# Kernel optimization log

Measured on AMD Instinct MI355X. Metric: run time of the kernel, lower is better.

Reference implementation:

```python
import jax, jax.numpy as jnp
import numpy as np

HEAD_DIM = 128
NUM_HEADS = 16
NUM_KV_HEADS = 16
ROPE_MAX_POS = 4096
ROPE_BASE = 10000.0


def _rope_tables(seq_len):
    # cos/sin cached tables: [S, D/2]
    inv_freq = 1.0 / (ROPE_BASE ** (jnp.arange(0, HEAD_DIM, 2, dtype=jnp.float32) / HEAD_DIM))
    t = jnp.arange(seq_len, dtype=jnp.float32)
    freqs = jnp.outer(t, inv_freq)
    return jnp.cos(freqs), jnp.sin(freqs)


def _apply_rope(x, cos, sin):
    # x: [B, S, H, D]; cos/sin: [S, D/2] -> broadcast over heads as [S, 1, D/2]
    orig_dtype = x.dtype
    c = cos[:, None, :]
    s = sin[:, None, :]
    xf = x.astype(jnp.float32)
    x_real, x_im = jnp.split(xf, 2, axis=-1)  # half-split (not interleaved) RoPE
    x_real_e = x_real * c - x_im * s
    x_im_e = x_im * c + x_real * s
    return jnp.concatenate((x_real_e, x_im_e), axis=-1).astype(orig_dtype)


def setup_inputs() -> dict:
    key = jax.random.key(0)
    k1, k2, k3 = jax.random.split(key, 3)
    B, S, H = 1, 4096, 2048
    hidden_states = jax.random.normal(k1, (B, S, H), dtype=jnp.float32)
    # trunc-normal-ish init, std ~ 1/sqrt(fan_in)
    w_qkv = jax.random.normal(k2, ((NUM_HEADS + 2 * NUM_KV_HEADS) * HEAD_DIM, H), dtype=jnp.float32) / jnp.sqrt(jnp.float32(H))
    w_o = jax.random.normal(k3, (H, NUM_HEADS * HEAD_DIM), dtype=jnp.float32) / jnp.sqrt(jnp.float32(NUM_HEADS * HEAD_DIM))
    return {"hidden_states": hidden_states, "w_qkv": w_qkv, "w_o": w_o}


def reference(hidden_states, w_qkv, w_o):
    B, S, _ = hidden_states.shape
    qkv = jnp.einsum('bsh,oh->bso', hidden_states, w_qkv)
    qkv = qkv.reshape(B, S, NUM_HEADS + 2 * NUM_KV_HEADS, HEAD_DIM)
    q = qkv[:, :, :NUM_HEADS]
    k = qkv[:, :, NUM_HEADS:NUM_HEADS + NUM_KV_HEADS]
    v = qkv[:, :, NUM_HEADS + NUM_KV_HEADS:]

    cos, sin = _rope_tables(S)
    q = _apply_rope(q, cos, sin)
    k = _apply_rope(k, cos, sin)

    scale = 1.0 / jnp.sqrt(jnp.float32(HEAD_DIM)).astype(q.dtype)
    # scores: [B, H, Sq, Sk]
    scores = jnp.einsum('bqhd,bkhd->bhqk', q, k) * scale
    causal = jnp.tril(jnp.ones((S, S), dtype=bool))
    scores = jnp.where(causal[None, None], scores, jnp.finfo(scores.dtype).min)
    probs = jax.nn.softmax(scores, axis=-1)
    attn = jnp.einsum('bhqk,bkhd->bqhd', probs, v)
    attn = attn.reshape(B, S, NUM_HEADS * HEAD_DIM)
    return jnp.einsum('bso,ho->bsh', attn, w_o)
```

## Files before the change

kernel.cpp:

```cpp
#include <hip/hip_runtime.h>

typedef __bf16 bf16;
typedef __bf16 bf16x8 __attribute__((ext_vector_type(8)));
typedef __bf16 bf16x4 __attribute__((ext_vector_type(4)));
typedef float f32x4 __attribute__((ext_vector_type(4)));

#define SEQ 4096
#define QKV_LD 6144
#define HNUM 16

__device__ __forceinline__ void async16(const bf16* g, bf16* l) {
    __builtin_amdgcn_global_load_lds((const __attribute__((address_space(1))) void*)g,
                                     (__attribute__((address_space(3))) void*)l, 16, 0, 0);
}

__global__ __launch_bounds__(256) void prep(const float* __restrict__ X, bf16* __restrict__ Xb,
                                            const float* __restrict__ Wq, bf16* __restrict__ Wqb,
                                            const float* __restrict__ Wo, bf16* __restrict__ Wob,
                                            float* __restrict__ T) {
    const int b = blockIdx.x, t = threadIdx.x;
    if (b < 12288) {
        const float* src;
        bf16* dst;
        int off;
        if (b < 4096)       { src = X;  dst = Xb;  off = b; }
        else if (b < 10240) { src = Wq; dst = Wqb; off = b - 4096; }
        else                { src = Wo; dst = Wob; off = b - 10240; }
        int i = (off * 256 + t) * 8;
        f32x4 a = *(const f32x4*)(src + i);
        f32x4 c = *(const f32x4*)(src + i + 4);
        bf16x8 w;
#pragma unroll
        for (int j = 0; j < 4; j++) { w[j] = (bf16)a[j]; w[4 + j] = (bf16)c[j]; }
        *(bf16x8*)(dst + i) = w;
    } else {
        int i = (b - 12288) * 256 + t;
        int s = i >> 6, d = i & 63;
        float inv_freq = powf(10000.0f, -(float)d * (1.0f / 64.0f));
        float ang = (float)s * inv_freq;
        T[2 * i]     = cosf(ang);
        T[2 * i + 1] = sinf(ang);
    }
}

__device__ __forceinline__ bf16x8 ldfrag(const bf16* slot, int row, int qd) {
    int lin  = row * 64 + qd * 16;
    int phys = lin ^ (((lin >> 9) & 1) << 5);
    return *(const bf16x8*)((const char*)slot + phys);
}

#define STAGE2(SG, SGR0, STT, SKK, SBUF, SMAT)                                  \
    {                                                                           \
        int tcl = (STT) < NT ? (STT) : NT - 1;                                  \
        const bf16* gsrc = (SG) + (size_t)(SGR0)*K + tcl * 64 + (SKK)*32;       \
        bf16* sl = &LDS[SBUF][SMAT][SKK][0];                                    \
        async16(gsrc + g0, (bf16*)((char*)sl + lb0));                           \
        async16(gsrc + g1, (bf16*)((char*)sl + lb1));                           \
    }

#define PHASE(QM, KKI, LOADB, SG, SGR0, STT, SKK, SBUF, SMAT, DOVM)             \
    {                                                                           \
        if (LOADB) {                                                            \
            _Pragma("unroll") for (int j = 0; j < 4; j++)                       \
                bB[j] = ldfrag(&LDS[bi][1][KKI][0], wc * 64 + j * 16 + ln, qd); \
        }                                                                       \
        bf16x8 aA[4];                                                           \
        _Pragma("unroll") for (int i = 0; i < 4; i++)                           \
            aA[i] = ldfrag(&LDS[bi][0][KKI][0],                                 \
                           wr * 128 + (QM)*64 + i * 16 + ln, qd);               \
        STAGE2(SG, SGR0, STT, SKK, SBUF, SMAT);                                 \
        __builtin_amdgcn_sched_barrier(0);                                      \
        if (DOVM) {                                                             \
            asm volatile("s_waitcnt vmcnt(4)" ::: "memory");                    \
            __builtin_amdgcn_sched_barrier(0);                                  \
        }                                                                       \
        __builtin_amdgcn_s_barrier();                                           \
        __builtin_amdgcn_sched_barrier(0);                                      \
        __builtin_amdgcn_s_setprio(1);                                          \
        _Pragma("unroll") for (int i = 0; i < 4; i++)                           \
            _Pragma("unroll") for (int j = 0; j < 4; j++)                       \
                acc[(QM)*4 + i][j] = __builtin_amdgcn_mfma_f32_16x16x32_bf16(   \
                    aA[i], bB[j], acc[(QM)*4 + i][j], 0, 0, 0);                 \
        __builtin_amdgcn_s_setprio(0);                                          \
        __builtin_amdgcn_sched_barrier(0);                                      \
        __builtin_amdgcn_s_barrier();                                           \
        __builtin_amdgcn_sched_barrier(0);                                      \
    }

__global__ __launch_bounds__(512, 2) void gemm256_nt(const bf16* __restrict__ A,
                                                     const bf16* __restrict__ B,
                                                     bf16* __restrict__ C,
                                                     int M, int N, int K) {
    __shared__ __align__(16) bf16 LDS[2][2][2][256 * 32];
    const int tid  = threadIdx.x;
    const int wave = tid >> 6, lane = tid & 63;
    const int qd = lane >> 4, ln = lane & 15;
    const int wr = wave >> 2, wc = wave & 3;
    const int bm = blockIdx.x * 256, bn = blockIdx.y * 256;
    const int NT = K >> 6;

    const int seg0 = wave * 2, seg1 = seg0 + 1;
    const int Pr0 = seg0 * 1024 + lane * 16;
    const int Pr1 = seg1 * 1024 + lane * 16;
    const int Lr0 = Pr0 ^ (((Pr0 >> 9) & 1) << 5);
    const int Lr1 = Pr1 ^ (((Pr1 >> 9) & 1) << 5);
    const size_t g0 = (size_t)(Lr0 >> 6) * K + ((Lr0 & 63) >> 1);
    const size_t g1 = (size_t)(Lr1 >> 6) * K + ((Lr1 & 63) >> 1);
    const int lb0 = seg0 * 1024, lb1 = seg1 * 1024;

    f32x4 acc[8][4] = {};

    STAGE2(A, bm, 0, 0, 0, 0);
    STAGE2(B, bn, 0, 0, 0, 1);
    STAGE2(A, bm, 0, 1, 0, 0);
    STAGE2(B, bn, 0, 1, 0, 1);
    STAGE2(A, bm, 1, 0, 1, 0);
    STAGE2(B, bn, 1, 0, 1, 1);
    __builtin_amdgcn_sched_barrier(0);
    asm volatile("s_waitcnt vmcnt(4)" ::: "memory");
    __builtin_amdgcn_sched_barrier(0);
    __builtin_amdgcn_s_barrier();
    __builtin_amdgcn_sched_barrier(0);

    for (int t = 0; t < NT; ++t) {
        const int bi = t & 1;
        bf16x8 bB[4];
        PHASE(0, 0, 1, A, bm, t + 1, 1, bi ^ 1, 0, 0)
        PHASE(1, 0, 0, B, bn, t + 1, 1, bi ^ 1, 1, 0)
        PHASE(0, 1, 1, A, bm, t + 2, 0, bi,     0, 0)
        PHASE(1, 1, 0, B, bn, t + 2, 0, bi,     1, 1)
    }
    asm volatile("s_waitcnt vmcnt(0)" ::: "memory");

    const size_t cb = (size_t)(bm + wr * 128 + qd * 4) * N + (bn + wc * 64 + ln);
#pragma unroll
    for (int mi = 0; mi < 8; mi++)
#pragma unroll
        for (int j = 0; j < 4; j++)
#pragma unroll
            for (int r = 0; r < 4; r++)
                C[cb + (size_t)(mi * 16 + r) * N + j * 16] = (bf16)acc[mi][j][r];
}

template <int A_F32, int B_F32, int C_F32>
__global__ __launch_bounds__(256) void gemm_nt(const void* __restrict__ Ap,
                                               const void* __restrict__ Bp,
                                               void* __restrict__ Cp,
                                               int M, int N, int K) {
    __shared__ __align__(16) bf16 sA[128 * 32];
    __shared__ __align__(16) bf16 sB[128 * 32];
    const int tid  = threadIdx.x;
    const int wave = tid >> 6, lane = tid & 63;
    const int qd = lane >> 4, ln = lane & 15;
    const int bm = blockIdx.x * 128, bn = blockIdx.y * 128;
    const int wm = (wave >> 1) * 64, wn = (wave & 1) * 64;

    const int srow = wave * 16 + (lane >> 2);
    const int scol = (lane & 3) * 8;
    const size_t rowoff = (size_t)srow * K + scol;
    const size_t rowskip = (size_t)64 * K;

    const bf16* Ab = (const bf16*)Ap + (size_t)bm * K + rowoff;
    const bf16* Bb = (const bf16*)Bp + (size_t)bn * K + rowoff;
    const float* Af = (const float*)Ap + (size_t)bm * K + rowoff;
    const float* Bf = (const float*)Bp + (size_t)bn * K + rowoff;
    bf16* sAd0 = &sA[(wave * 16) * 32];
    bf16* sAd1 = &sA[(64 + wave * 16) * 32];
    bf16* sBd0 = &sB[(wave * 16) * 32];
    bf16* sBd1 = &sB[(64 + wave * 16) * 32];
    bf16* sAw0 = &sA[srow * 32 + scol];
    bf16* sAw1 = &sA[(64 + srow) * 32 + scol];
    bf16* sBw0 = &sB[srow * 32 + scol];
    bf16* sBw1 = &sB[(64 + srow) * 32 + scol];

    f32x4 acc[4][4] = {};
    for (int k0 = 0; k0 < K; k0 += 32) {
        if (A_F32) {
            f32x4 u0 = *(const f32x4*)(Af + k0);
            f32x4 u1 = *(const f32x4*)(Af + k0 + 4);
            f32x4 u2 = *(const f32x4*)(Af + rowskip + k0);
            f32x4 u3 = *(const f32x4*)(Af + rowskip + k0 + 4);
            bf16x8 w0, w1;
#pragma unroll
            for (int i = 0; i < 4; i++) { w0[i] = (bf16)u0[i]; w0[4 + i] = (bf16)u1[i];
                                          w1[i] = (bf16)u2[i]; w1[4 + i] = (bf16)u3[i]; }
            *(bf16x8*)sAw0 = w0;
            *(bf16x8*)sAw1 = w1;
        } else {
            async16(Ab + k0, sAd0);
            async16(Ab + rowskip + k0, sAd1);
        }
        if (B_F32) {
            f32x4 u0 = *(const f32x4*)(Bf + k0);
            f32x4 u1 = *(const f32x4*)(Bf + k0 + 4);
            f32x4 u2 = *(const f32x4*)(Bf + rowskip + k0);
            f32x4 u3 = *(const f32x4*)(Bf + rowskip + k0 + 4);
            bf16x8 w0, w1;
#pragma unroll
            for (int i = 0; i < 4; i++) { w0[i] = (bf16)u0[i]; w0[4 + i] = (bf16)u1[i];
                                          w1[i] = (bf16)u2[i]; w1[4 + i] = (bf16)u3[i]; }
            *(bf16x8*)sBw0 = w0;
            *(bf16x8*)sBw1 = w1;
        } else {
            async16(Bb + k0, sBd0);
            async16(Bb + rowskip + k0, sBd1);
        }
        __syncthreads();
        bf16x8 af[4], bfr[4];
#pragma unroll
        for (int i = 0; i < 4; i++)
            af[i] = *(const bf16x8*)&sA[(wm + i * 16 + ln) * 32 + qd * 8];
#pragma unroll
        for (int j = 0; j < 4; j++)
            bfr[j] = *(const bf16x8*)&sB[(wn + j * 16 + ln) * 32 + qd * 8];
#pragma unroll
        for (int i = 0; i < 4; i++)
#pragma unroll
            for (int j = 0; j < 4; j++)
                acc[i][j] = __builtin_amdgcn_mfma_f32_16x16x32_bf16(af[i], bfr[j], acc[i][j], 0, 0, 0);
        __syncthreads();
    }
    const size_t cbase = (size_t)(bm + wm + qd * 4) * N + (bn + wn + ln);
#pragma unroll
    for (int i = 0; i < 4; i++)
#pragma unroll
        for (int j = 0; j < 4; j++)
#pragma unroll
            for (int r = 0; r < 4; r++) {
                size_t idx = cbase + (size_t)(i * 16 + r) * N + j * 16;
                if (C_F32) ((float*)Cp)[idx] = acc[i][j][r];
                else       ((bf16*)Cp)[idx] = (bf16)acc[i][j][r];
            }
}

__global__ __launch_bounds__(256) void rope_tv(bf16* __restrict__ QKV,
                                               const float* __restrict__ T,
                                               bf16* __restrict__ VT) {
    __shared__ bf16 tl[64][65];
    const int b = blockIdx.x, t = threadIdx.x;
    if (b < 4096) {
        const int s  = b;
        const int hh = t >> 3;
        const int d0 = (t & 7) * 8;
        bf16* p = QKV + (size_t)s * QKV_LD + hh * 128 + d0;
        bf16x8 x0 = *(const bf16x8*)(p);
        bf16x8 x1 = *(const bf16x8*)(p + 64);
        const float2* Tb = (const float2*)T + (size_t)s * 64 + d0;
        bf16x8 y0, y1;
#pragma unroll
        for (int e = 0; e < 8; e++) {
            float2 cs = Tb[e];
            float a = (float)x0[e], c = (float)x1[e];
            y0[e] = (bf16)(a * cs.x - c * cs.y);
            y1[e] = (bf16)(c * cs.x + a * cs.y);
        }
        *(bf16x8*)(p)      = y0;
        *(bf16x8*)(p + 64) = y1;
    } else {
        const int b2 = b - 4096;
        const int s0 = (b2 & 63) * 64;
        const int d0 = (b2 >> 6) * 64;
        const int r = t >> 3, c = t & 7;
#pragma unroll
        for (int u = 0; u < 2; u++) {
            bf16x8 v = *(const bf16x8*)(QKV + (size_t)(s0 + u * 32 + r) * QKV_LD + 4096 + d0 + c * 8);
#pragma unroll
            for (int e = 0; e < 8; e++) tl[u * 32 + r][c * 8 + e] = v[e];
        }
        __syncthreads();
#pragma unroll
        for (int u = 0; u < 2; u++) {
            bf16x8 w;
#pragma unroll
            for (int e = 0; e < 8; e++) w[e] = tl[c * 8 + e][u * 32 + r];
            *(bf16x8*)(VT + (size_t)(d0 + u * 32 + r) * SEQ + s0 + c * 8) = w;
        }
    }
}

__global__ __launch_bounds__(256) void rope_k_inline(bf16* __restrict__ QKV) {
    const int s  = blockIdx.x;
    const int t  = threadIdx.x;
    const int hh = (blockIdx.y << 2) + (t >> 6);
    const int d  = t & 63;
    bf16* p = QKV + (size_t)s * QKV_LD + hh * 128 + d;
    float x0 = (float)p[0];
    float x1 = (float)p[64];
    float inv_freq = powf(10000.0f, -(float)d * (1.0f / 64.0f));
    float ang = (float)s * inv_freq;
    float c = cosf(ang), sn = sinf(ang);
    p[0]  = (bf16)(x0 * c - x1 * sn);
    p[64] = (bf16)(x1 * c + x0 * sn);
}

template <int USE_VT>
__global__ __launch_bounds__(256, 2) void flash_attn(const bf16* __restrict__ QKV,
                                                     const bf16* __restrict__ VT,
                                                     bf16* __restrict__ O) {
    __shared__ __align__(16) bf16 sK[64 * 128];
    __shared__ __align__(16) bf16 sV[128 * 64];
    __shared__ __align__(16) bf16 sP[4][32 * 64];
    const int tid  = threadIdx.x;
    const int wave = tid >> 6, lane = tid & 63;
    const int qd = lane >> 4, ln = lane & 15;
    const int h  = blockIdx.x;
    const int y  = blockIdx.y;
    const int qtile = (y < 16) ? (31 - y) : (y - 16);
    const int qw0 = qtile * 128 + wave * 32;
    const int nkv = 2 * qtile + 2;
    const float scale = 0.08838834764831843f;

    bf16x8 Qf[2][4];
#pragma unroll
    for (int qt = 0; qt < 2; qt++) {
        const bf16* Qg = QKV + (size_t)(qw0 + qt * 16 + ln) * QKV_LD + h * 128;
#pragma unroll
        for (int ks = 0; ks < 4; ks++) {
            bf16x8 q8 = *(const bf16x8*)(Qg + ks * 32 + qd * 8);
#pragma unroll
            for (int e = 0; e < 8; e++) q8[e] = (bf16)((float)q8[e] * scale);
            Qf[qt][ks] = q8;
        }
    }

    f32x4 Oacc[2][8] = {};
    float l_i[2] = {0.0f, 0.0f};

    const int krow = tid >> 4;
    const int kblk = tid & 15;
    const int vrow = tid >> 3;
    const int vblk = tid & 7;
    const int vd   = tid & 127;
    const int vh   = tid >> 7;
    const bf16* Kg  = QKV + 2048 + h * 128;
    const bf16* Vg  = QKV + 4096 + h * 128;
    const bf16* VTg = VT + (size_t)h * 128 * SEQ;

    bf16x8 Kpre[4], Vpre[4];
#pragma unroll
    for (int rr = 0; rr < 4; rr++)
        Kpre[rr] = *(const bf16x8*)(Kg + (size_t)(rr * 16 + krow) * QKV_LD + kblk * 8);
    if (USE_VT) {
#pragma unroll
        for (int u = 0; u < 4; u++)
            Vpre[u] = *(const bf16x8*)(VTg + (size_t)(u * 32 + vrow) * SEQ + vblk * 8);
    } else {
#pragma unroll
        for (int u = 0; u < 4; u++)
#pragma unroll
            for (int j = 0; j < 8; j++)
                Vpre[u][j] = Vg[(size_t)(vh * 32 + u * 8 + j) * QKV_LD + vd];
    }

    for (int kt = 0; kt < nkv; kt++) {
        const int kbase = kt * 64;
#pragma unroll
        for (int rr = 0; rr < 4; rr++) {
            int kv = rr * 16 + krow;
            *(bf16x8*)&sK[kv * 128 + ((kblk ^ (kv & 7)) * 8)] = Kpre[rr];
        }
        if (USE_VT) {
#pragma unroll
            for (int u = 0; u < 4; u++) {
                int d = u * 32 + vrow;
                *(bf16x8*)&sV[d * 64 + ((vblk ^ (d & 7)) * 8)] = Vpre[u];
            }
        } else {
#pragma unroll
            for (int u = 0; u < 4; u++)
                *(bf16x8*)&sV[vd * 64 + (((vh * 4 + u) ^ (vd & 7)) * 8)] = Vpre[u];
        }
        __syncthreads();
        if (kt + 1 < nkv) {
            const int nb = kbase + 64;
#pragma unroll
            for (int rr = 0; rr < 4; rr++)
                Kpre[rr] = *(const bf16x8*)(Kg + (size_t)(nb + rr * 16 + krow) * QKV_LD + kblk * 8);
            if (USE_VT) {
#pragma unroll
                for (int u = 0; u < 4; u++)
                    Vpre[u] = *(const bf16x8*)(VTg + (size_t)(u * 32 + vrow) * SEQ + nb + vblk * 8);
            } else {
#pragma unroll
                for (int u = 0; u < 4; u++)
#pragma unroll
                    for (int j = 0; j < 8; j++)
                        Vpre[u][j] = Vg[(size_t)(nb + vh * 32 + u * 8 + j) * QKV_LD + vd];
            }
        }
        if (kbase <= qw0 + 31) {
            f32x4 Sacc[2][4] = {};
#pragma unroll
            for (int ks = 0; ks < 4; ks++)
#pragma unroll
                for (int j = 0; j < 4; j++) {
                    bf16x8 af = *(const bf16x8*)&sK[(j * 16 + ln) * 128 + (((ks * 4 + qd) ^ (ln & 7)) * 8)];
                    Sacc[0][j] = __builtin_amdgcn_mfma_f32_16x16x32_bf16(af, Qf[0][ks], Sacc[0][j], 0, 0, 0);
                    Sacc[1][j] = __builtin_amdgcn_mfma_f32_16x16x32_bf16(af, Qf[1][ks], Sacc[1][j], 0, 0, 0);
                }
#pragma unroll
            for (int qt = 0; qt < 2; qt++) {
                const int qs = qw0 + qt * 16;
                if (kbase + 63 > qs) {
#pragma unroll
                    for (int j = 0; j < 4; j++)
#pragma unroll
                        for (int r = 0; r < 4; r++)
                            if (kbase + j * 16 + qd * 4 + r > qs + ln) Sacc[qt][j][r] = -1e30f;
                }
                float psum = 0.0f;
#pragma unroll
                for (int j = 0; j < 4; j++) {
                    bf16x4 p4;
#pragma unroll
                    for (int r = 0; r < 4; r++) {
                        float p = __expf(Sacc[qt][j][r]);
                        psum += p;
                        p4[r] = (bf16)p;
                    }
                    int blk = (j * 2 + (qd >> 1)) ^ (ln & 7);
                    *(bf16x4*)&sP[wave][(qt * 16 + ln) * 64 + blk * 8 + (qd & 1) * 4] = p4;
                }
                psum += __shfl_xor(psum, 16);
                psum += __shfl_xor(psum, 32);
                l_i[qt] += psum;
            }
#pragma unroll
            for (int ks = 0; ks < 2; ks++) {
                bf16x8 pf0 = *(const bf16x8*)&sP[wave][(0 * 16 + ln) * 64 + (((ks * 4 + qd) ^ (ln & 7)) * 8)];
                bf16x8 pf1 = *(const bf16x8*)&sP[wave][(1 * 16 + ln) * 64 + (((ks * 4 + qd) ^ (ln & 7)) * 8)];
#pragma unroll
                for (int dt = 0; dt < 8; dt++) {
                    bf16x8 vf = *(const bf16x8*)&sV[(dt * 16 + ln) * 64 + (((ks * 4 + qd) ^ (ln & 7)) * 8)];
                    Oacc[0][dt] = __builtin_amdgcn_mfma_f32_16x16x32_bf16(pf0, vf, Oacc[0][dt], 0, 0, 0);
                    Oacc[1][dt] = __builtin_amdgcn_mfma_f32_16x16x32_bf16(pf1, vf, Oacc[1][dt], 0, 0, 0);
                }
            }
        }
        __syncthreads();
    }
#pragma unroll
    for (int qt = 0; qt < 2; qt++) {
        float linv[4];
#pragma unroll
        for (int r = 0; r < 4; r++)
            linv[r] = 1.0f / __shfl(l_i[qt], (lane & 48) | (qd * 4 + r));
        bf16* Ob = O + (size_t)(qw0 + qt * 16 + qd * 4) * 2048 + h * 128 + ln;
#pragma unroll
        for (int dt = 0; dt < 8; dt++)
#pragma unroll
            for (int r = 0; r < 4; r++)
                Ob[(size_t)r * 2048 + dt * 16] = (bf16)(Oacc[qt][dt][r] * linv[r]);
    }
}

extern "C" void kernel_launch(void* const* d_in, const int* in_sizes, int n_in,
                              void* d_out, int out_size, void* d_ws, size_t ws_size,
                              hipStream_t stream) {
    const float* X    = (const float*)d_in[0];
    const float* Wqkv = (const float*)d_in[1];
    const float* Wo   = (const float*)d_in[2];
    float* out = (float*)d_out;
    bf16* QKV = (bf16*)d_ws;
    bf16* ATT = QKV + (size_t)4096 * 6144;

    const size_t nX = (size_t)4096 * 2048, nWq = (size_t)6144 * 2048, nWo = (size_t)2048 * 2048;
    const size_t need = (nX * 3 + nWq * 2 + nWo) * 2 + nX * 2;

    if (ws_size >= need) {
        bf16* Xb  = ATT + nX;
        bf16* Wqb = Xb + nX;
        bf16* Wob = Wqb + nWq;
        bf16*  VT  = Xb;
        float* Tab = (float*)ATT;
        prep<<<13312, 256, 0, stream>>>(X, Xb, Wqkv, Wqb, Wo, Wob, Tab);
        gemm256_nt<<<dim3(16, 24), 512, 0, stream>>>(Xb, Wqb, QKV, 4096, 6144, 2048);
        rope_tv<<<6144, 256, 0, stream>>>(QKV, Tab, VT);
        flash_attn<1><<<dim3(HNUM, 32), 256, 0, stream>>>(QKV, VT, ATT);
        gemm_nt<0, 0, 1><<<dim3(32, 16), 256, 0, stream>>>(ATT, Wob, out, 4096, 2048, 2048);
    } else {
        gemm_nt<1, 1, 0><<<dim3(32, 48), 256, 0, stream>>>(X, Wqkv, QKV, 4096, 6144, 2048);
        rope_k_inline<<<dim3(4096, 8), 256, 0, stream>>>(QKV);
        flash_attn<0><<<dim3(HNUM, 32), 256, 0, stream>>>(QKV, (const bf16*)nullptr, ATT);
        gemm_nt<0, 1, 1><<<dim3(32, 16), 256, 0, stream>>>(ATT, Wo, out, 4096, 2048, 2048);
    }
}
```

Measured before the change: 430.4 us.

## Switch QKV and output GEMMs to a 128x256 pipelined MFMA kernel

Replaces the 256x256 QKV projection kernel with a templated 128x256 variant that keeps the same async LDS double-buffered pipeline, with fewer accumulators and two phases per k-tile. The smaller tile doubles the block count for the QKV GEMM (768 blocks instead of 384), aiming for better CU fill and less wave quantization. The same kernel, now able to write fp32 output, also replaces the simpler 128x128 output-projection GEMM. In exchange, the QKV GEMM loses some per-block reuse of its operands.

After: 416.4 us. -3.3%, faster.

```diff
diff --git a/kernel.cpp b/kernel.cpp
--- a/kernel.cpp
+++ b/kernel.cpp
@@ -43,103 +43,103 @@
     }
 }
 
+
 __device__ __forceinline__ bf16x8 ldfrag(const bf16* slot, int row, int qd) {
     int lin  = row * 64 + qd * 16;
     int phys = lin ^ (((lin >> 9) & 1) << 5);
     return *(const bf16x8*)((const char*)slot + phys);
 }
 
-#define STAGE2(SG, SGR0, STT, SKK, SBUF, SMAT)                                  \
-    {                                                                           \
-        int tcl = (STT) < NT ? (STT) : NT - 1;                                  \
-        const bf16* gsrc = (SG) + (size_t)(SGR0)*K + tcl * 64 + (SKK)*32;       \
-        bf16* sl = &LDS[SBUF][SMAT][SKK][0];                                    \
-        async16(gsrc + g0, (bf16*)((char*)sl + lb0));                           \
-        async16(gsrc + g1, (bf16*)((char*)sl + lb1));                           \
-    }
-
-#define PHASE(QM, KKI, LOADB, SG, SGR0, STT, SKK, SBUF, SMAT, DOVM)             \
-    {                                                                           \
-        if (LOADB) {                                                            \
-            _Pragma("unroll") for (int j = 0; j < 4; j++)                       \
-                bB[j] = ldfrag(&LDS[bi][1][KKI][0], wc * 64 + j * 16 + ln, qd); \
-        }                                                                       \
-        bf16x8 aA[4];                                                           \
-        _Pragma("unroll") for (int i = 0; i < 4; i++)                           \
-            aA[i] = ldfrag(&LDS[bi][0][KKI][0],                                 \
-                           wr * 128 + (QM)*64 + i * 16 + ln, qd);               \
-        STAGE2(SG, SGR0, STT, SKK, SBUF, SMAT);                                 \
-        __builtin_amdgcn_sched_barrier(0);                                      \
-        if (DOVM) {                                                             \
-            asm volatile("s_waitcnt vmcnt(4)" ::: "memory");                    \
-            __builtin_amdgcn_sched_barrier(0);                                  \
-        }                                                                       \
-        __builtin_amdgcn_s_barrier();                                           \
-        __builtin_amdgcn_sched_barrier(0);                                      \
-        __builtin_amdgcn_s_setprio(1);                                          \
-        _Pragma("unroll") for (int i = 0; i < 4; i++)                           \
-            _Pragma("unroll") for (int j = 0; j < 4; j++)                       \
-                acc[(QM)*4 + i][j] = __builtin_amdgcn_mfma_f32_16x16x32_bf16(   \
-                    aA[i], bB[j], acc[(QM)*4 + i][j], 0, 0, 0);                 \
-        __builtin_amdgcn_s_setprio(0);                                          \
-        __builtin_amdgcn_sched_barrier(0);                                      \
-        __builtin_amdgcn_s_barrier();                                           \
-        __builtin_amdgcn_sched_barrier(0);                                      \
-    }
-
-__global__ __launch_bounds__(512, 2) void gemm256_nt(const bf16* __restrict__ A,
-                                                     const bf16* __restrict__ B,
-                                                     bf16* __restrict__ C,
-                                                     int M, int N, int K) {
-    __shared__ __align__(16) bf16 LDS[2][2][2][256 * 32];
+#define STG(TT, KKI, BUF)                                                      \
+    {                                                                          \
+        int tcl = (TT) < NT ? (TT) : NT - 1;                                   \
+        const bf16* As = A + (size_t)bm * K + tcl * 64 + (KKI)*32;             \
+        const bf16* Bs = B + (size_t)bn * K + tcl * 64 + (KKI)*32;             \
+        async16(As + gA,  (bf16*)((char*)&LA[BUF][KKI][0] + lbA));             \
+        async16(Bs + gB0, (bf16*)((char*)&LB[BUF][KKI][0] + lbB0));            \
+        async16(Bs + gB1, (bf16*)((char*)&LB[BUF][KKI][0] + lbB1));            \
+    }
+
+#define PH(KKI, TT, SKK, SBUF, DOVM)                                           \
+    {                                                                          \
+        bf16x8 aA[4], bB[4];                                                   \
+        _Pragma("unroll") for (int i = 0; i < 4; i++)                          \
+            aA[i] = ldfrag(&LA[bi][KKI][0], wr * 64 + i * 16 + ln, qd);        \
+        _Pragma("unroll") for (int j = 0; j < 4; j++)                          \
+            bB[j] = ldfrag(&LB[bi][KKI][0], wc * 64 + j * 16 + ln, qd);        \
+        STG(TT, SKK, SBUF);                                                    \
+        __builtin_amdgcn_sched_barrier(0);                                     \
+        if (DOVM) {                                                            \
+            asm volatile("s_waitcnt vmcnt(3)" ::: "memory");                   \
+            __builtin_amdgcn_sched_barrier(0);                                 \
+        }                                                                      \
+        __builtin_amdgcn_s_barrier();                                          \
+        __builtin_amdgcn_sched_barrier(0);                                     \
+        __builtin_amdgcn_s_setprio(1);                                         \
+        _Pragma("unroll") for (int i = 0; i < 4; i++)                          \
+            _Pragma("unroll") for (int j = 0; j < 4; j++)                      \
+                acc[i][j] = __builtin_amdgcn_mfma_f32_16x16x32_bf16(           \
+                    aA[i], bB[j], acc[i][j], 0, 0, 0);                         \
+        __builtin_amdgcn_s_setprio(0);                                         \
+        __builtin_amdgcn_sched_barrier(0);                                     \
+        __builtin_amdgcn_s_barrier();                                          \
+        __builtin_amdgcn_sched_barrier(0);                                     \
+    }
+
+template <int C_F32>
+__global__ __launch_bounds__(512, 2) void gemm128x256(const bf16* __restrict__ A,
+                                                      const bf16* __restrict__ B,
+                                                      void* __restrict__ Cp,
+                                                      int M, int N, int K) {
+    __shared__ __align__(16) bf16 LA[2][2][128 * 32];
+    __shared__ __align__(16) bf16 LB[2][2][256 * 32];
     const int tid  = threadIdx.x;
     const int wave = tid >> 6, lane = tid & 63;
     const int qd = lane >> 4, ln = lane & 15;
     const int wr = wave >> 2, wc = wave & 3;
-    const int bm = blockIdx.x * 256, bn = blockIdx.y * 256;
+    const int bm = blockIdx.x * 128, bn = blockIdx.y * 256;
     const int NT = K >> 6;
 
-    const int seg0 = wave * 2, seg1 = seg0 + 1;
-    const int Pr0 = seg0 * 1024 + lane * 16;
-    const int Pr1 = seg1 * 1024 + lane * 16;
-    const int Lr0 = Pr0 ^ (((Pr0 >> 9) & 1) << 5);
-    const int Lr1 = Pr1 ^ (((Pr1 >> 9) & 1) << 5);
-    const size_t g0 = (size_t)(Lr0 >> 6) * K + ((Lr0 & 63) >> 1);
-    const size_t g1 = (size_t)(Lr1 >> 6) * K + ((Lr1 & 63) >> 1);
-    const int lb0 = seg0 * 1024, lb1 = seg1 * 1024;
-
-    f32x4 acc[8][4] = {};
-
-    STAGE2(A, bm, 0, 0, 0, 0);
-    STAGE2(B, bn, 0, 0, 0, 1);
-    STAGE2(A, bm, 0, 1, 0, 0);
-    STAGE2(B, bn, 0, 1, 0, 1);
-    STAGE2(A, bm, 1, 0, 1, 0);
-    STAGE2(B, bn, 1, 0, 1, 1);
+    const int PrA  = wave * 1024 + lane * 16;
+    const int PrB0 = (2 * wave) * 1024 + lane * 16;
+    const int PrB1 = PrB0 + 1024;
+    const int LrA  = PrA  ^ (((PrA  >> 9) & 1) << 5);
+    const int LrB0 = PrB0 ^ (((PrB0 >> 9) & 1) << 5);
+    const int LrB1 = PrB1 ^ (((PrB1 >> 9) & 1) << 5);
+    const size_t gA  = (size_t)(LrA  >> 6) * K + ((LrA  & 63) >> 1);
+    const size_t gB0 = (size_t)(LrB0 >> 6) * K + ((LrB0 & 63) >> 1);
+    const size_t gB1 = (size_t)(LrB1 >> 6) * K + ((LrB1 & 63) >> 1);
+    const int lbA = wave * 1024, lbB0 = 2 * wave * 1024, lbB1 = lbB0 + 1024;
+
+    f32x4 acc[4][4] = {};
+
+    STG(0, 0, 0);
+    STG(0, 1, 0);
+    STG(1, 0, 1);
     __builtin_amdgcn_sched_barrier(0);
-    asm volatile("s_waitcnt vmcnt(4)" ::: "memory");
+    asm volatile("s_waitcnt vmcnt(3)" ::: "memory");
     __builtin_amdgcn_sched_barrier(0);
     __builtin_amdgcn_s_barrier();
     __builtin_amdgcn_sched_barrier(0);
 
     for (int t = 0; t < NT; ++t) {
         const int bi = t & 1;
-        bf16x8 bB[4];
-        PHASE(0, 0, 1, A, bm, t + 1, 1, bi ^ 1, 0, 0)
-        PHASE(1, 0, 0, B, bn, t + 1, 1, bi ^ 1, 1, 0)
-        PHASE(0, 1, 1, A, bm, t + 2, 0, bi,     0, 0)
-        PHASE(1, 1, 0, B, bn, t + 2, 0, bi,     1, 1)
+        PH(0, t + 1, 1, bi ^ 1, 0)
+        PH(1, t + 2, 0, bi,     1)
     }
     asm volatile("s_waitcnt vmcnt(0)" ::: "memory");
 
-    const size_t cb = (size_t)(bm + wr * 128 + qd * 4) * N + (bn + wc * 64 + ln);
-#pragma unroll
-    for (int mi = 0; mi < 8; mi++)
+    const size_t cb = (size_t)(bm + wr * 64 + qd * 4) * N + (bn + wc * 64 + ln);
+#pragma unroll
+    for (int mi = 0; mi < 4; mi++)
 #pragma unroll
         for (int j = 0; j < 4; j++)
 #pragma unroll
-            for (int r = 0; r < 4; r++)
-                C[cb + (size_t)(mi * 16 + r) * N + j * 16] = (bf16)acc[mi][j][r];
+            for (int r = 0; r < 4; r++) {
+                size_t idx = cb + (size_t)(mi * 16 + r) * N + j * 16;
+                if (C_F32) ((float*)Cp)[idx] = acc[mi][j][r];
+                else       ((bf16*)Cp)[idx]  = (bf16)acc[mi][j][r];
+            }
 }
 
 template <int A_F32, int B_F32, int C_F32>
@@ -474,10 +474,10 @@
         bf16*  VT  = Xb;
         float* Tab = (float*)ATT;
         prep<<<13312, 256, 0, stream>>>(X, Xb, Wqkv, Wqb, Wo, Wob, Tab);
-        gemm256_nt<<<dim3(16, 24), 512, 0, stream>>>(Xb, Wqb, QKV, 4096, 6144, 2048);
+        gemm128x256<0><<<dim3(32, 24), 512, 0, stream>>>(Xb, Wqb, QKV, 4096, 6144, 2048);
         rope_tv<<<6144, 256, 0, stream>>>(QKV, Tab, VT);
         flash_attn<1><<<dim3(HNUM, 32), 256, 0, stream>>>(QKV, VT, ATT);
-        gemm_nt<0, 0, 1><<<dim3(32, 16), 256, 0, stream>>>(ATT, Wob, out, 4096, 2048, 2048);
+        gemm128x256<1><<<dim3(32, 8), 512, 0, stream>>>(ATT, Wob, out, 4096, 2048, 2048);
     } else {
         gemm_nt<1, 1, 0><<<dim3(32, 48), 256, 0, stream>>>(X, Wqkv, QKV, 4096, 6144, 2048);
         rope_k_inline<<<dim3(4096, 8), 256, 0, stream>>>(QKV);
```
